# Kernel tuning notes

Measured on AMD Instinct MI355X. Metric: run time of the kernel, lower is better.

Reference implementation:

```python
import jax, jax.numpy as jnp
import numpy as np

B, N, K, D = 256, 100, 16, 128


def setup_inputs() -> dict:
    key = jax.random.key(0)
    k1, k2, k3, k4, k5, k6, k7 = jax.random.split(key, 7)
    return {
        "self_vectors": jax.random.normal(k1, (B, N, D), jnp.float32),
        "neighbor_vector": jax.random.normal(k2, (B, N, K, D), jnp.float32),
        "neighbor_weight": jax.random.uniform(k3, (B, N, K), jnp.float32),
        "extra_vector": jax.random.normal(k4, (B, N, D), jnp.float32),
        "w_1": jax.random.normal(k5, (D + 1, D), jnp.float32) / np.sqrt(D + 1),
        "w_2": jax.random.normal(k6, (D, 1), jnp.float32) / np.sqrt(D),
        "w_3": jax.random.normal(k7, (2 * D, D), jnp.float32) / np.sqrt(2 * D),
        "batch_size": B,
    }


def reference(self_vectors, neighbor_vector, neighbor_weight, extra_vector, w_1, w_2, w_3, batch_size):
    # attention branch (extra_vector is not None)
    feat = extra_vector[:, :, None, :] * neighbor_vector           # [B,N,K,D]
    feat = jnp.concatenate([feat, neighbor_weight[..., None]], -1)  # [B,N,K,D+1]
    alpha = jnp.einsum('bnkf,fd->bnkd', feat, w_1)                  # [B,N,K,D]
    alpha = jax.nn.leaky_relu(alpha, negative_slope=0.2)
    alpha = jnp.einsum('bnkd,do->bnk', alpha, w_2)                  # [B,N,K]
    alpha = jax.nn.softmax(alpha, axis=-1)[..., None]               # [B,N,K,1]
    agg = jnp.sum(alpha * neighbor_vector, axis=-2)                 # [B,N,D]
    # combine (dropout is identity in eval mode / p=0)
    out = jnp.concatenate([self_vectors, agg], axis=-1) @ w_3       # [B,N,D]
    out = out.reshape(batch_size, -1, w_3.shape[1])
    return jax.nn.relu(out)
```

## Files before the change

kernel.cpp:

```cpp
#include <hip/hip_runtime.h>
#include <stdint.h>

#define BN_TOTAL 25600
#define DDIM 128
#define KN 16

typedef __bf16 bf16x8 __attribute__((ext_vector_type(8)));
typedef float f32x4 __attribute__((ext_vector_type(4)));
typedef float f32x16 __attribute__((ext_vector_type(16)));

__device__ __forceinline__ void gload_lds16(const void* g, void* l) {
    __builtin_amdgcn_global_load_lds(
        (const __attribute__((address_space(1))) void*)g,
        (__attribute__((address_space(3))) void*)l, 16, 0, 0);
}

__global__ __launch_bounds__(256) void k0_build_frags(
    const float* __restrict__ w1,
    const float* __restrict__ w3,
    bf16x8* __restrict__ fw1,
    bf16x8* __restrict__ fw3)
{
    const int slot = blockIdx.x * 256 + threadIdx.x;
    if (slot < 2048) {
        const int idx  = slot >> 6;
        const int lane = slot & 63;
        const int t = idx >> 2, s = idx & 3;
        const int grp = lane >> 4, lr = lane & 15;
        const int fbase = grp * 8 + 32 * s;
        const int d = t * 16 + lr;
        bf16x8 tmp;
        #pragma unroll
        for (int j = 0; j < 8; ++j)
            tmp[j] = (__bf16)w1[(fbase + j) * DDIM + d];
        fw1[slot] = tmp;
    } else {
        const int q = slot - 2048;
        const int idx  = q >> 6;
        const int lane = q & 63;
        const int t = idx >> 3, s = idx & 7;
        const int grp = lane >> 4, lr = lane & 15;
        const int fbase = grp * 8 + 32 * s;
        const int d = t * 16 + lr;
        bf16x8 tmp;
        #pragma unroll
        for (int j = 0; j < 8; ++j)
            tmp[j] = (__bf16)w3[(fbase + j) * DDIM + d];
        fw3[q] = tmp;
    }
}

__global__ __launch_bounds__(256) void k1_attn_agg(
    const float* __restrict__ nbr,
    const float* __restrict__ wgt,
    const float* __restrict__ extra,
    const float* __restrict__ w1,
    const float* __restrict__ w2,
    const bf16x8* __restrict__ fw1,
    unsigned short* __restrict__ aggb)
{
    __shared__ bf16x8 b1frag[32][64];
    __shared__ float w1last[DDIM];
    __shared__ float w2s[DDIM];

    const int tid  = threadIdx.x;
    const int lane = tid & 63;
    const int wave = tid >> 6;
    const int grp  = lane >> 4;
    const int lr   = lane & 15;
    const int half = lane >> 5;
    const int col  = lane & 31;

    const int bn = blockIdx.x * 4 + wave;
    const float* nb = nbr   + (size_t)bn * (KN * DDIM);
    const float* ex = extra + (size_t)bn * DDIM;

    const float4 wv   = *(const float4*)(wgt + (size_t)bn * KN + grp * 4);
    const float4 p_n0 = *(const float4*)(nb + lr * DDIM + grp * 8);
    const float4 p_n1 = *(const float4*)(nb + lr * DDIM + grp * 8 + 4);
    const float4 p_e0 = *(const float4*)(ex + grp * 8);
    const float4 p_e1 = *(const float4*)(ex + grp * 8 + 4);

    #pragma unroll
    for (int c = 0; c < 8; ++c)
        gload_lds16(fw1 + (wave * 8 + c) * 64 + lane, &b1frag[wave * 8 + c][0]);
    if (tid < DDIM) {
        w1last[tid] = w1[DDIM * DDIM + tid];
        w2s[tid]    = w2[tid];
    }
    __syncthreads();

    f32x4 acc[8];
    #pragma unroll
    for (int t = 0; t < 8; ++t) {
        const float wl = w1last[t * 16 + lr];
        acc[t][0] = wv.x * wl;
        acc[t][1] = wv.y * wl;
        acc[t][2] = wv.z * wl;
        acc[t][3] = wv.w * wl;
    }

    #pragma unroll
    for (int s = 0; s < 4; ++s) {
        const int f0 = grp * 8 + 32 * s;
        float4 n0, n1, e0, e1;
        if (s == 0) { n0 = p_n0; n1 = p_n1; e0 = p_e0; e1 = p_e1; }
        else {
            n0 = *(const float4*)(nb + lr * DDIM + f0);
            n1 = *(const float4*)(nb + lr * DDIM + f0 + 4);
            e0 = *(const float4*)(ex + f0);
            e1 = *(const float4*)(ex + f0 + 4);
        }
        bf16x8 af;
        af[0] = (__bf16)(n0.x * e0.x); af[1] = (__bf16)(n0.y * e0.y);
        af[2] = (__bf16)(n0.z * e0.z); af[3] = (__bf16)(n0.w * e0.w);
        af[4] = (__bf16)(n1.x * e1.x); af[5] = (__bf16)(n1.y * e1.y);
        af[6] = (__bf16)(n1.z * e1.z); af[7] = (__bf16)(n1.w * e1.w);
        #pragma unroll
        for (int t = 0; t < 8; ++t)
            acc[t] = __builtin_amdgcn_mfma_f32_16x16x32_bf16(af, b1frag[t * 4 + s][lane], acc[t], 0, 0, 0);
    }

    bf16x8 b2f[4];
    #pragma unroll
    for (int t = 0; t < 4; ++t)
        #pragma unroll
        for (int j = 0; j < 8; ++j)
            b2f[t][j] = (__bf16)nb[(half * 8 + j) * DDIM + t * 32 + col];

    float sum0 = 0.f, sum1 = 0.f, sum2 = 0.f, sum3 = 0.f;
    #pragma unroll
    for (int t = 0; t < 8; ++t) {
        const float w2v = w2s[t * 16 + lr];
        float h;
        h = acc[t][0]; h = fmaxf(h, 0.2f * h); sum0 = fmaf(h, w2v, sum0);
        h = acc[t][1]; h = fmaxf(h, 0.2f * h); sum1 = fmaf(h, w2v, sum1);
        h = acc[t][2]; h = fmaxf(h, 0.2f * h); sum2 = fmaf(h, w2v, sum2);
        h = acc[t][3]; h = fmaxf(h, 0.2f * h); sum3 = fmaf(h, w2v, sum3);
    }
    #pragma unroll
    for (int m = 1; m <= 8; m <<= 1) {
        sum0 += __shfl_xor(sum0, m, 64);
        sum1 += __shfl_xor(sum1, m, 64);
        sum2 += __shfl_xor(sum2, m, 64);
        sum3 += __shfl_xor(sum3, m, 64);
    }
    float mx = fmaxf(fmaxf(sum0, sum1), fmaxf(sum2, sum3));
    mx = fmaxf(mx, __shfl_xor(mx, 16, 64));
    mx = fmaxf(mx, __shfl_xor(mx, 32, 64));
    const float ev0 = __expf(sum0 - mx);
    const float ev1 = __expf(sum1 - mx);
    const float ev2 = __expf(sum2 - mx);
    const float ev3 = __expf(sum3 - mx);
    float es = ev0 + ev1 + ev2 + ev3;
    es += __shfl_xor(es, 16, 64);
    es += __shfl_xor(es, 32, 64);
    const float inv = 1.0f / es;

    bf16x8 a2;
    #pragma unroll
    for (int j = 0; j < 8; ++j) {
        const int src = (((half * 8 + j) >> 2) << 4);
        float av;
        switch (j & 3) {
            case 0: av = __shfl(ev0, src, 64); break;
            case 1: av = __shfl(ev1, src, 64); break;
            case 2: av = __shfl(ev2, src, 64); break;
            default: av = __shfl(ev3, src, 64); break;
        }
        a2[j] = (__bf16)(av * inv);
    }

    f32x16 z;
    #pragma unroll
    for (int i = 0; i < 16; ++i) z[i] = 0.f;

    unsigned short* ao = aggb + (size_t)bn * DDIM;
    #pragma unroll
    for (int t = 0; t < 4; ++t) {
        const f32x16 r = __builtin_amdgcn_mfma_f32_32x32x16_bf16(a2, b2f[t], z, 0, 0, 0);
        if (lane < 32) {
            const __bf16 rb = (__bf16)r[0];
            ao[t * 32 + col] = __builtin_bit_cast(unsigned short, rb);
        }
    }
}

__global__ __launch_bounds__(64) void k2_out_gemm(
    const float* __restrict__ selfv,
    const unsigned short* __restrict__ aggb,
    const bf16x8* __restrict__ fw3,
    float* __restrict__ out)
{
    const int lane = threadIdx.x;
    const int grp  = lane >> 4;
    const int lr   = lane & 15;
    const int rowbase = blockIdx.x * 16;
    const int row = rowbase + lr;

    f32x4 acc[8];
    #pragma unroll
    for (int t = 0; t < 8; ++t) {
        acc[t][0] = 0.f; acc[t][1] = 0.f; acc[t][2] = 0.f; acc[t][3] = 0.f;
    }

    const bf16x8* fp = fw3 + lane;
    #pragma unroll
    for (int s = 0; s < 8; ++s) {
        bf16x8 af;
        if (s < 4) {
            const int f0 = grp * 8 + 32 * s;
            const float4 x0 = *(const float4*)(selfv + (size_t)row * DDIM + f0);
            const float4 x1 = *(const float4*)(selfv + (size_t)row * DDIM + f0 + 4);
            af[0] = (__bf16)x0.x; af[1] = (__bf16)x0.y;
            af[2] = (__bf16)x0.z; af[3] = (__bf16)x0.w;
            af[4] = (__bf16)x1.x; af[5] = (__bf16)x1.y;
            af[6] = (__bf16)x1.z; af[7] = (__bf16)x1.w;
        } else {
            const int f0 = grp * 8 + 32 * (s - 4);
            af = *(const bf16x8*)(aggb + (size_t)row * DDIM + f0);
        }
        #pragma unroll
        for (int t = 0; t < 8; ++t)
            acc[t] = __builtin_amdgcn_mfma_f32_16x16x32_bf16(af, fp[(t * 8 + s) * 64], acc[t], 0, 0, 0);
    }

    #pragma unroll
    for (int t = 0; t < 8; ++t) {
        #pragma unroll
        for (int j = 0; j < 4; ++j) {
            const int r = rowbase + grp * 4 + j;
            out[(size_t)r * DDIM + t * 16 + lr] = fmaxf(acc[t][j], 0.0f);
        }
    }
}

extern "C" void kernel_launch(void* const* d_in, const int* in_sizes, int n_in,
                              void* d_out, int out_size, void* d_ws, size_t ws_size,
                              hipStream_t stream)
{
    const float* selfv = (const float*)d_in[0];
    const float* nbr   = (const float*)d_in[1];
    const float* wgt   = (const float*)d_in[2];
    const float* extra = (const float*)d_in[3];
    const float* w1    = (const float*)d_in[4];
    const float* w2    = (const float*)d_in[5];
    const float* w3    = (const float*)d_in[6];
    float* out = (float*)d_out;

    unsigned short* aggb = (unsigned short*)d_ws;
    bf16x8* fw1 = (bf16x8*)((char*)d_ws + (8u << 20));
    bf16x8* fw3 = (bf16x8*)((char*)d_ws + (8u << 20) + (128u << 10));

    hipLaunchKernelGGL(k0_build_frags, dim3(24), dim3(256), 0, stream, w1, w3, fw1, fw3);
    hipLaunchKernelGGL(k1_attn_agg, dim3(6400), dim3(256), 0, stream,
                       nbr, wgt, extra, w1, w2, fw1, aggb);
    hipLaunchKernelGGL(k2_out_gemm, dim3(1600), dim3(64), 0, stream,
                       selfv, aggb, fw3, out);
}
```

Baseline: 75.29 us.

## Loop k1 over several rows per wave and stage W3 fragments in LDS

k1 now processes five (b,n) rows per wave in a loop, amortizing the per-block LDS load of W1 fragments and the w1last/w2 register setup across more work, with grid reduced accordingly. k2 becomes a 256-thread block that loads all W3 fragments into LDS once and serves four waves, instead of each 64-thread block reading fragments from global memory. The aggregate store now splits columns across both half-waves. The trade-off is fewer blocks, which reduces latency hiding in the memory-bound k1, and the prefetch of the first neighbor chunk before the barrier is dropped.

```diff
diff --git a/kernel.cpp b/kernel.cpp
--- a/kernel.cpp
+++ b/kernel.cpp
@@ -50,6 +50,7 @@
     }
 }
 
+#define K1_ITERS 5
 __global__ __launch_bounds__(256) void k1_attn_agg(
     const float* __restrict__ nbr,
     const float* __restrict__ wgt,
@@ -71,16 +72,6 @@
     const int half = lane >> 5;
     const int col  = lane & 31;
 
-    const int bn = blockIdx.x * 4 + wave;
-    const float* nb = nbr   + (size_t)bn * (KN * DDIM);
-    const float* ex = extra + (size_t)bn * DDIM;
-
-    const float4 wv   = *(const float4*)(wgt + (size_t)bn * KN + grp * 4);
-    const float4 p_n0 = *(const float4*)(nb + lr * DDIM + grp * 8);
-    const float4 p_n1 = *(const float4*)(nb + lr * DDIM + grp * 8 + 4);
-    const float4 p_e0 = *(const float4*)(ex + grp * 8);
-    const float4 p_e1 = *(const float4*)(ex + grp * 8 + 4);
-
     #pragma unroll
     for (int c = 0; c < 8; ++c)
         gload_lds16(fw1 + (wave * 8 + c) * 64 + lane, &b1frag[wave * 8 + c][0]);
@@ -90,112 +81,133 @@
     }
     __syncthreads();
 
-    f32x4 acc[8];
+    float wl[8], w2v[8];
     #pragma unroll
     for (int t = 0; t < 8; ++t) {
-        const float wl = w1last[t * 16 + lr];
-        acc[t][0] = wv.x * wl;
-        acc[t][1] = wv.y * wl;
-        acc[t][2] = wv.z * wl;
-        acc[t][3] = wv.w * wl;
-    }
-
-    #pragma unroll
-    for (int s = 0; s < 4; ++s) {
-        const int f0 = grp * 8 + 32 * s;
-        float4 n0, n1, e0, e1;
-        if (s == 0) { n0 = p_n0; n1 = p_n1; e0 = p_e0; e1 = p_e1; }
-        else {
-            n0 = *(const float4*)(nb + lr * DDIM + f0);
-            n1 = *(const float4*)(nb + lr * DDIM + f0 + 4);
-            e0 = *(const float4*)(ex + f0);
-            e1 = *(const float4*)(ex + f0 + 4);
-        }
-        bf16x8 af;
-        af[0] = (__bf16)(n0.x * e0.x); af[1] = (__bf16)(n0.y * e0.y);
-        af[2] = (__bf16)(n0.z * e0.z); af[3] = (__bf16)(n0.w * e0.w);
-        af[4] = (__bf16)(n1.x * e1.x); af[5] = (__bf16)(n1.y * e1.y);
-        af[6] = (__bf16)(n1.z * e1.z); af[7] = (__bf16)(n1.w * e1.w);
-        #pragma unroll
-        for (int t = 0; t < 8; ++t)
-            acc[t] = __builtin_amdgcn_mfma_f32_16x16x32_bf16(af, b1frag[t * 4 + s][lane], acc[t], 0, 0, 0);
-    }
-
-    bf16x8 b2f[4];
-    #pragma unroll
-    for (int t = 0; t < 4; ++t)
-        #pragma unroll
-        for (int j = 0; j < 8; ++j)
-            b2f[t][j] = (__bf16)nb[(half * 8 + j) * DDIM + t * 32 + col];
-
-    float sum0 = 0.f, sum1 = 0.f, sum2 = 0.f, sum3 = 0.f;
-    #pragma unroll
-    for (int t = 0; t < 8; ++t) {
-        const float w2v = w2s[t * 16 + lr];
-        float h;
-        h = acc[t][0]; h = fmaxf(h, 0.2f * h); sum0 = fmaf(h, w2v, sum0);
-        h = acc[t][1]; h = fmaxf(h, 0.2f * h); sum1 = fmaf(h, w2v, sum1);
-        h = acc[t][2]; h = fmaxf(h, 0.2f * h); sum2 = fmaf(h, w2v, sum2);
-        h = acc[t][3]; h = fmaxf(h, 0.2f * h); sum3 = fmaf(h, w2v, sum3);
-    }
-    #pragma unroll
-    for (int m = 1; m <= 8; m <<= 1) {
-        sum0 += __shfl_xor(sum0, m, 64);
-        sum1 += __shfl_xor(sum1, m, 64);
-        sum2 += __shfl_xor(sum2, m, 64);
-        sum3 += __shfl_xor(sum3, m, 64);
-    }
-    float mx = fmaxf(fmaxf(sum0, sum1), fmaxf(sum2, sum3));
-    mx = fmaxf(mx, __shfl_xor(mx, 16, 64));
-    mx = fmaxf(mx, __shfl_xor(mx, 32, 64));
-    const float ev0 = __expf(sum0 - mx);
-    const float ev1 = __expf(sum1 - mx);
-    const float ev2 = __expf(sum2 - mx);
-    const float ev3 = __expf(sum3 - mx);
-    float es = ev0 + ev1 + ev2 + ev3;
-    es += __shfl_xor(es, 16, 64);
-    es += __shfl_xor(es, 32, 64);
-    const float inv = 1.0f / es;
-
-    bf16x8 a2;
-    #pragma unroll
-    for (int j = 0; j < 8; ++j) {
-        const int src = (((half * 8 + j) >> 2) << 4);
-        float av;
-        switch (j & 3) {
-            case 0: av = __shfl(ev0, src, 64); break;
-            case 1: av = __shfl(ev1, src, 64); break;
-            case 2: av = __shfl(ev2, src, 64); break;
-            default: av = __shfl(ev3, src, 64); break;
-        }
-        a2[j] = (__bf16)(av * inv);
-    }
-
-    f32x16 z;
-    #pragma unroll
-    for (int i = 0; i < 16; ++i) z[i] = 0.f;
-
-    unsigned short* ao = aggb + (size_t)bn * DDIM;
-    #pragma unroll
-    for (int t = 0; t < 4; ++t) {
-        const f32x16 r = __builtin_amdgcn_mfma_f32_32x32x16_bf16(a2, b2f[t], z, 0, 0, 0);
-        if (lane < 32) {
-            const __bf16 rb = (__bf16)r[0];
-            ao[t * 32 + col] = __builtin_bit_cast(unsigned short, rb);
-        }
-    }
-}
-
-__global__ __launch_bounds__(64) void k2_out_gemm(
+        wl[t]  = w1last[t * 16 + lr];
+        w2v[t] = w2s[t * 16 + lr];
+    }
+
+    const int base = (blockIdx.x * 4 + wave) * K1_ITERS;
+
+    for (int it = 0; it < K1_ITERS; ++it) {
+        const int bn = base + it;
+        const float* nb = nbr   + (size_t)bn * (KN * DDIM);
+        const float* ex = extra + (size_t)bn * DDIM;
+
+        const float4 wv = *(const float4*)(wgt + (size_t)bn * KN + grp * 4);
+        f32x4 acc[8];
+        #pragma unroll
+        for (int t = 0; t < 8; ++t) {
+            acc[t][0] = wv.x * wl[t];
+            acc[t][1] = wv.y * wl[t];
+            acc[t][2] = wv.z * wl[t];
+            acc[t][3] = wv.w * wl[t];
+        }
+
+        #pragma unroll
+        for (int s = 0; s < 4; ++s) {
+            const int f0 = grp * 8 + 32 * s;
+            const float4 n0 = *(const float4*)(nb + lr * DDIM + f0);
+            const float4 n1 = *(const float4*)(nb + lr * DDIM + f0 + 4);
+            const float4 e0 = *(const float4*)(ex + f0);
+            const float4 e1 = *(const float4*)(ex + f0 + 4);
+            bf16x8 af;
+            af[0] = (__bf16)(n0.x * e0.x); af[1] = (__bf16)(n0.y * e0.y);
+            af[2] = (__bf16)(n0.z * e0.z); af[3] = (__bf16)(n0.w * e0.w);
+            af[4] = (__bf16)(n1.x * e1.x); af[5] = (__bf16)(n1.y * e1.y);
+            af[6] = (__bf16)(n1.z * e1.z); af[7] = (__bf16)(n1.w * e1.w);
+            #pragma unroll
+            for (int t = 0; t < 8; ++t)
+                acc[t] = __builtin_amdgcn_mfma_f32_16x16x32_bf16(
+                             af, b1frag[t * 4 + s][lane], acc[t], 0, 0, 0);
+        }
+
+        bf16x8 b2f[4];
+        #pragma unroll
+        for (int t = 0; t < 4; ++t)
+            #pragma unroll
+            for (int j = 0; j < 8; ++j)
+                b2f[t][j] = (__bf16)nb[(half * 8 + j) * DDIM + t * 32 + col];
+
+        float sum0 = 0.f, sum1 = 0.f, sum2 = 0.f, sum3 = 0.f;
+        #pragma unroll
+        for (int t = 0; t < 8; ++t) {
+            float h;
+            h = acc[t][0]; h = fmaxf(h, 0.2f * h); sum0 = fmaf(h, w2v[t], sum0);
+            h = acc[t][1]; h = fmaxf(h, 0.2f * h); sum1 = fmaf(h, w2v[t], sum1);
+            h = acc[t][2]; h = fmaxf(h, 0.2f * h); sum2 = fmaf(h, w2v[t], sum2);
+            h = acc[t][3]; h = fmaxf(h, 0.2f * h); sum3 = fmaf(h, w2v[t], sum3);
+        }
+        #pragma unroll
+        for (int m = 1; m <= 8; m <<= 1) {
+            sum0 += __shfl_xor(sum0, m, 64);
+            sum1 += __shfl_xor(sum1, m, 64);
+            sum2 += __shfl_xor(sum2, m, 64);
+            sum3 += __shfl_xor(sum3, m, 64);
+        }
+        float mx = fmaxf(fmaxf(sum0, sum1), fmaxf(sum2, sum3));
+        mx = fmaxf(mx, __shfl_xor(mx, 16, 64));
+        mx = fmaxf(mx, __shfl_xor(mx, 32, 64));
+        const float ev0 = __expf(sum0 - mx);
+        const float ev1 = __expf(sum1 - mx);
+        const float ev2 = __expf(sum2 - mx);
+        const float ev3 = __expf(sum3 - mx);
+        float es = ev0 + ev1 + ev2 + ev3;
+        es += __shfl_xor(es, 16, 64);
+        es += __shfl_xor(es, 32, 64);
+        const float inv = 1.0f / es;
+
+        bf16x8 a2;
+        #pragma unroll
+        for (int j = 0; j < 8; ++j) {
+            const int src = (((half * 8 + j) >> 2) << 4);
+            float av;
+            switch (j & 3) {
+                case 0: av = __shfl(ev0, src, 64); break;
+                case 1: av = __shfl(ev1, src, 64); break;
+                case 2: av = __shfl(ev2, src, 64); break;
+                default: av = __shfl(ev3, src, 64); break;
+            }
+            a2[j] = (__bf16)(av * inv);
+        }
+
+        f32x16 z;
+        #pragma unroll
+        for (int i = 0; i < 16; ++i) z[i] = 0.f;
+
+        unsigned short* ao = aggb + (size_t)bn * DDIM;
+        #pragma unroll
+        for (int t = 0; t < 4; ++t) {
+            const f32x16 r = __builtin_amdgcn_mfma_f32_32x32x16_bf16(a2, b2f[t], z, 0, 0, 0);
+            if ((t >> 1) == half) {
+                const __bf16 rb = (__bf16)r[0];
+                ao[t * 32 + col] = __builtin_bit_cast(unsigned short, rb);
+            }
+        }
+    }
+}
+
+__global__ __launch_bounds__(256) void k2_out_gemm(
     const float* __restrict__ selfv,
     const unsigned short* __restrict__ aggb,
     const bf16x8* __restrict__ fw3,
     float* __restrict__ out)
 {
-    const int lane = threadIdx.x;
+    __shared__ bf16x8 w3frag[64][64];
+
+    const int tid  = threadIdx.x;
+    const int lane = tid & 63;
+    const int wave = tid >> 6;
     const int grp  = lane >> 4;
     const int lr   = lane & 15;
-    const int rowbase = blockIdx.x * 16;
+
+    #pragma unroll
+    for (int c = 0; c < 16; ++c)
+        gload_lds16(fw3 + (wave * 16 + c) * 64 + lane, &w3frag[wave * 16 + c][0]);
+    __syncthreads();
+
+    const int rowbase = blockIdx.x * 64 + wave * 16;
     const int row = rowbase + lr;
 
     f32x4 acc[8];
@@ -204,7 +216,6 @@
         acc[t][0] = 0.f; acc[t][1] = 0.f; acc[t][2] = 0.f; acc[t][3] = 0.f;
     }
 
-    const bf16x8* fp = fw3 + lane;
     #pragma unroll
     for (int s = 0; s < 8; ++s) {
         bf16x8 af;
@@ -222,7 +233,7 @@
         }
         #pragma unroll
         for (int t = 0; t < 8; ++t)
-            acc[t] = __builtin_amdgcn_mfma_f32_16x16x32_bf16(af, fp[(t * 8 + s) * 64], acc[t], 0, 0, 0);
+            acc[t] = __builtin_amdgcn_mfma_f32_16x16x32_bf16(af, w3frag[t * 8 + s][lane], acc[t], 0, 0, 0);
     }
 
     #pragma unroll
@@ -253,8 +264,8 @@
     bf16x8* fw3 = (bf16x8*)((char*)d_ws + (8u << 20) + (128u << 10));
 
     hipLaunchKernelGGL(k0_build_frags, dim3(24), dim3(256), 0, stream, w1, w3, fw1, fw3);
-    hipLaunchKernelGGL(k1_attn_agg, dim3(6400), dim3(256), 0, stream,
+    hipLaunchKernelGGL(k1_attn_agg, dim3(1280), dim3(256), 0, stream,
                        nbr, wgt, extra, w1, w2, fw1, aggb);
-    hipLaunchKernelGGL(k2_out_gemm, dim3(1600), dim3(64), 0, stream,
+    hipLaunchKernelGGL(k2_out_gemm, dim3(400), dim3(256), 0, stream,
                        selfv, aggb, fw3, out);
 }
```

Result: slower. 114.0 us (+51.4%).
